# Kernel tuning notes

Measured on AMD Instinct MI355X. Metric: run time of the kernel, lower is better.

The kernel has to match this reference:

```python
import jax, jax.numpy as jnp
import numpy as np

HOP = 512
FAC = 4
FRAME_LEN = FAC * HOP  # 2048
ALPHA = 0.65
BETA = 0.06


def _inverse_stft_window():
    # torch.hann_window (periodic): w[n] = 0.5*(1 - cos(2*pi*n/N))
    n = np.arange(FRAME_LEN)
    w = 0.5 * (1.0 - np.cos(2.0 * np.pi * n / FRAME_LEN))
    denom = w ** 2
    # overlaps = ceil(frame_length / hop) == FAC (frame_length = FAC*HOP exactly)
    denom = denom.reshape(FAC, HOP).sum(axis=0)          # [HOP]
    denom = np.tile(denom, FAC)                          # [FRAME_LEN]
    return (w / denom).astype(np.float32)


def setup_inputs() -> dict:
    key = jax.random.key(0)
    B, F, T = 8, 1024, 2048
    stft_frames = jax.random.normal(key, (B, 2, F, T), dtype=jnp.float32)
    inv_window = jnp.asarray(_inverse_stft_window())
    return {"stft_frames": stft_frames, "inv_window": inv_window}


def reference(stft_frames, inv_window):
    # stft_frames: [B, 2, F, T] (real/imag stacked on dim 1)
    x = jnp.pad(stft_frames, ((0, 0), (0, 0), (0, 1), (0, 0)))  # F -> F+1 (Nyquist bin)
    real = x[:, 0] / BETA   # [B, F+1, T]
    imag = x[:, 1] / BETA
    # denormalize_complex: |x|^(1/alpha) * exp(i * atan2(im, re))
    mag = (real * real + imag * imag) ** (0.5 / ALPHA)
    theta = jnp.arctan2(imag, real)
    spec = jax.lax.complex(mag * jnp.cos(theta), mag * jnp.sin(theta))  # [B, F+1, T]
    frames = jnp.fft.irfft(spec, axis=-2)                 # [B, 2F, T], 2F == FRAME_LEN
    frames = jnp.transpose(frames, (0, 2, 1))             # [B, T, L]
    frames = frames * inv_window[None, None, :]
    B, T, L = frames.shape
    total = (T - 1) * HOP + L
    # vectorized overlap-add (scatter-add replacing the per-frame python loop)
    idx = (jnp.arange(T)[:, None] * HOP + jnp.arange(L)[None, :]).reshape(-1)  # [T*L]
    full = jnp.zeros((B, total), frames.dtype).at[:, idx].add(frames.reshape(B, -1))
    # output_buffer is empty on the first call; chunk = first hop*T samples
    return full[:, : HOP * T]
```

## Files before the change

### kernel.cpp

```cpp
#include <hip/hip_runtime.h>
#include <cstddef>


#define TDIM 2048
#define FDIM 1024
#define TT 8
#define NTOT (512 * 2048)
#define SPLANE 4224

static constexpr int kBREV[32] = {0,16,8,24,4,20,12,28,2,18,10,26,6,22,14,30,
                                  1,17,9,25,5,21,13,29,3,19,11,27,7,23,15,31};
static constexpr float kTR[16] = {
  1.0f, 0.98078528040323044f, 0.92387953251128674f, 0.83146961230254524f,
  0.70710678118654757f, 0.55557023301960218f, 0.38268343236508978f, 0.19509032201612825f,
  0.0f, -0.19509032201612825f, -0.38268343236508978f, -0.55557023301960218f,
  -0.70710678118654757f, -0.83146961230254524f, -0.92387953251128674f, -0.98078528040323044f};
static constexpr float kTI[16] = {
  0.0f, 0.19509032201612825f, 0.38268343236508978f, 0.55557023301960218f,
  0.70710678118654757f, 0.83146961230254524f, 0.92387953251128674f, 0.98078528040323044f,
  1.0f, 0.98078528040323044f, 0.92387953251128674f, 0.83146961230254524f,
  0.70710678118654757f, 0.55557023301960218f, 0.38268343236508978f, 0.19509032201612825f};
static constexpr float kCC[32] = {
  1.0f, 0.99518472667219693f, 0.98078528040323044f, 0.95694033573220882f,
  0.92387953251128674f, 0.88192126434835505f, 0.83146961230254524f, 0.77301045336273699f,
  0.70710678118654757f, 0.63439328416364549f, 0.55557023301960218f, 0.47139673682599764f,
  0.38268343236508978f, 0.29028467725446233f, 0.19509032201612825f, 0.098017140329560604f,
  0.0f, -0.098017140329560604f, -0.19509032201612825f, -0.29028467725446233f,
  -0.38268343236508978f, -0.47139673682599764f, -0.55557023301960218f, -0.63439328416364549f,
  -0.70710678118654757f, -0.77301045336273699f, -0.83146961230254524f, -0.88192126434835505f,
  -0.92387953251128674f, -0.95694033573220882f, -0.98078528040323044f, -0.99518472667219693f};
static constexpr float kSS[32] = {
  0.0f, 0.098017140329560604f, 0.19509032201612825f, 0.29028467725446233f,
  0.38268343236508978f, 0.47139673682599764f, 0.55557023301960218f, 0.63439328416364549f,
  0.70710678118654757f, 0.77301045336273699f, 0.83146961230254524f, 0.88192126434835505f,
  0.92387953251128674f, 0.95694033573220882f, 0.98078528040323044f, 0.99518472667219693f,
  1.0f, 0.99518472667219693f, 0.98078528040323044f, 0.95694033573220882f,
  0.92387953251128674f, 0.88192126434835505f, 0.83146961230254524f, 0.77301045336273699f,
  0.70710678118654757f, 0.63439328416364549f, 0.55557023301960218f, 0.47139673682599764f,
  0.38268343236508978f, 0.29028467725446233f, 0.19509032201612825f, 0.098017140329560604f};

template <int H>
__device__ __forceinline__ void fft32_stage(float ar[32], float ai[32]) {
  constexpr int TSTEP = 16 / H;
  #pragma unroll
  for (int g = 0; g < 32; g += 2 * H) {
    #pragma unroll
    for (int j = 0; j < H; ++j) {
      const float twr = kTR[j * TSTEP];
      const float twi = kTI[j * TSTEP];
      const int i0 = g + j, i1 = i0 + H;
      const float tr = twr * ar[i1] - twi * ai[i1];
      const float ti = twr * ai[i1] + twi * ar[i1];
      ar[i1] = ar[i0] - tr; ai[i1] = ai[i0] - ti;
      ar[i0] += tr;         ai[i0] += ti;
    }
  }
}

__device__ __forceinline__ void ifft32_core(float ar[32], float ai[32]) {
  fft32_stage<1>(ar, ai);
  fft32_stage<2>(ar, ai);
  fft32_stage<4>(ar, ai);
  fft32_stage<8>(ar, ai);
  fft32_stage<16>(ar, ai);
}

__device__ __forceinline__ float pow_gain(float v, float PE, float KS) {
  return KS * __builtin_amdgcn_exp2f(PE * __builtin_amdgcn_logf(v));
}

__device__ __forceinline__ void denorm4(float4& r, float4& i, float PE, float KS) {
  float g;
  g = pow_gain(r.x * r.x + i.x * i.x, PE, KS); r.x *= g; i.x *= g;
  g = pow_gain(r.y * r.y + i.y * i.y, PE, KS); r.y *= g; i.y *= g;
  g = pow_gain(r.z * r.z + i.z * i.z, PE, KS); r.z *= g; i.z *= g;
  g = pow_gain(r.w * r.w + i.w * i.w, PE, KS); r.w *= g; i.w *= g;
}

template <int SC>
__device__ __forceinline__ int slot_row(int s) {
  return (SC == 0) ? (s < 256 ? s : s + 512) : (s + 256);
}

template <int SC>
__device__ __forceinline__ void stage1_compute(const float* __restrict__ Sre,
                                               const float* __restrict__ Sim,
                                               int q, int tl, float wc, float ws,
                                               float ar[32], float ai[32]) {
  #pragma unroll
  for (int u = 0; u < 16; ++u) {
    const int k2 = (SC == 0) ? (u < 8 ? u : u + 16) : (u + 8);
    const int slot = q + 32 * u;
    int slotm_zero = 32 * (16 - u);
    if (SC == 0 && u == 0) slotm_zero = 0;
    if (SC == 0 && u == 8) slotm_zero = 512;
    const int slotm_pos = (32 - q) + 32 * (15 - u);
    const int slotm = (q == 0) ? slotm_zero : slotm_pos;

    const float s1r = Sre[slot * 8 + tl],  s1i = Sim[slot * 8 + tl];
    const float s2r = Sre[slotm * 8 + tl], s2i = Sim[slotm * 8 + tl];
    const float cs = wc * kCC[k2] - ws * kSS[k2];
    const float sn = ws * kCC[k2] + wc * kSS[k2];
    const float Pre = s1r + s2r, Pim = s1i - s2i;
    const float Qre = s1r - s2r, Qim = s1i + s2i;
    const float uu = cs * Qim + sn * Qre;
    const float vv = cs * Qre - sn * Qim;
    float wr = Pre - uu, wi = Pim + vv;
    if (q == 0 && k2 == 0) { wr = s1r; wi = s1r; }
    ar[kBREV[k2]] = wr; ai[kBREV[k2]] = wi;
  }
}

#define XIDX(t, k1, r) ((k1) * 264 + (r) * 8 + (t))
#define FSTR 2054

__global__ __launch_bounds__(256) void istft_fused(const float* __restrict__ in,
                                                   const float* __restrict__ invw,
                                                   float* __restrict__ out) {
  __shared__ float buf[16896];
  float* Sre = buf;
  float* Sim = buf + SPLANE;
  float* Xr  = buf;
  float* Xi  = buf + 8448;
  float* Fh  = buf;

  const int tid = threadIdx.x;
  const int tl  = tid & 7;
  const int q   = tid >> 3;

  const int id   = blockIdx.x;
  const int xcd  = id & 7;
  const int slot = id >> 3;
  const int b    = slot >> 5;
  const int tile = xcd * 32 + (slot & 31);
  const int t0   = tile * TT;

  const float* re_p = in + ((size_t)b * 2 + 0) * ((size_t)FDIM * TDIM);
  const float* im_p = in + ((size_t)b * 2 + 1) * ((size_t)FDIM * TDIM);

  const float KS = (float)(exp((-1.0 / 0.65) * log(0.06)) / 2048.0);
  const float PE = 7.0f / 26.0f;

  const float aq = 3.0679615757712824e-3f * (float)q;
  const float wc = __cosf(aq), ws = __sinf(aq);

  float ar[32], ai[32];

  {
    float4 reA[4], imA[4];
    #pragma unroll
    for (int j = 0; j < 4; ++j) {
      const int f = tid + 256 * j;
      const int s = f >> 1, cg = f & 1;
      const int row = slot_row<0>(s);
      reA[j] = *(const float4*)(re_p + (size_t)row * TDIM + t0 + 4 * cg);
      imA[j] = *(const float4*)(im_p + (size_t)row * TDIM + t0 + 4 * cg);
    }
    float4 exRe, exIm;
    if (tid < 2) {
      exRe = *(const float4*)(re_p + (size_t)256 * TDIM + t0 + 4 * tid);
      exIm = *(const float4*)(im_p + (size_t)256 * TDIM + t0 + 4 * tid);
    }
    #pragma unroll
    for (int j = 0; j < 4; ++j) {
      const int f = tid + 256 * j;
      const int s = f >> 1, cg = f & 1;
      denorm4(reA[j], imA[j], PE, KS);
      *(float4*)(Sre + s * 8 + 4 * cg) = reA[j];
      *(float4*)(Sim + s * 8 + 4 * cg) = imA[j];
    }
    if (tid < 2) {
      denorm4(exRe, exIm, PE, KS);
      *(float4*)(Sre + 512 * 8 + 4 * tid) = exRe;
      *(float4*)(Sim + 512 * 8 + 4 * tid) = exIm;
    }

    float4 reB[4], imB[4];
    #pragma unroll
    for (int j = 0; j < 4; ++j) {
      const int f = tid + 256 * j;
      const int s = f >> 1, cg = f & 1;
      const int row = slot_row<1>(s);
      reB[j] = *(const float4*)(re_p + (size_t)row * TDIM + t0 + 4 * cg);
      imB[j] = *(const float4*)(im_p + (size_t)row * TDIM + t0 + 4 * cg);
    }
    float4 exReB, exImB;
    if (tid < 2) {
      exReB = *(const float4*)(re_p + (size_t)768 * TDIM + t0 + 4 * tid);
      exImB = *(const float4*)(im_p + (size_t)768 * TDIM + t0 + 4 * tid);
    }
    __syncthreads();

    stage1_compute<0>(Sre, Sim, q, tl, wc, ws, ar, ai);
    __syncthreads();

    #pragma unroll
    for (int j = 0; j < 4; ++j) {
      const int f = tid + 256 * j;
      const int s = f >> 1, cg = f & 1;
      denorm4(reB[j], imB[j], PE, KS);
      *(float4*)(Sre + s * 8 + 4 * cg) = reB[j];
      *(float4*)(Sim + s * 8 + 4 * cg) = imB[j];
    }
    if (tid < 2) {
      denorm4(exReB, exImB, PE, KS);
      *(float4*)(Sre + 512 * 8 + 4 * tid) = exReB;
      *(float4*)(Sim + 512 * 8 + 4 * tid) = exImB;
    }
    __syncthreads();
    stage1_compute<1>(Sre, Sim, q, tl, wc, ws, ar, ai);
    __syncthreads();
  }

  ifft32_core(ar, ai);

  {
    const float aq2 = 6.1359231515425649e-3f * (float)q;
    const float dc = __cosf(aq2), dsn = __sinf(aq2);
    float cs = 1.0f, sn = 0.0f;
    #pragma unroll
    for (int r = 0; r < 32; ++r) {
      Xr[XIDX(tl, q, r)] = cs * ar[r] - sn * ai[r];
      Xi[XIDX(tl, q, r)] = cs * ai[r] + sn * ar[r];
      const float ncs = cs * dc - sn * dsn;
      sn = cs * dsn + sn * dc;
      cs = ncs;
    }
  }
  __syncthreads();
  float zr[32], zi[32];
  #pragma unroll
  for (int i = 0; i < 32; ++i) {
    zr[i] = Xr[XIDX(tl, kBREV[i], q)];
    zi[i] = Xi[XIDX(tl, kBREV[i], q)];
  }
  __syncthreads();

  ifft32_core(zr, zi);

  #pragma unroll
  for (int s = 0; s < 32; ++s) {
    const int l0 = 2 * q + 64 * s;
    const float2 w2 = *(const float2*)(invw + l0);
    float2 fv; fv.x = zr[s] * w2.x; fv.y = zi[s] * w2.y;
    *(float2*)(Fh + tl * FSTR + l0) = fv;
  }
  __syncthreads();

  float* ob = out + (size_t)b * NTOT;
  for (int rel = 0; rel < 11; ++rel) {
    const int tp = t0 + rel;
    if (tp > 2047) break;
    #pragma unroll
    for (int half = 0; half < 2; ++half) {
      const int j = tid + 256 * half;
      float v = 0.0f;
      #pragma unroll
      for (int c = 0; c < 4; ++c) {
        const int tt = rel - c;
        if (tt >= 0 && tt < TT) v += Fh[tt * FSTR + j + 512 * c];
      }
      const int n = tp * 512 + j;
      if (rel >= 3 && rel <= 7) ob[n] = v;
      else atomicAdd(&ob[n], v);
    }
  }
}

extern "C" void kernel_launch(void* const* d_in, const int* in_sizes, int n_in,
                              void* d_out, int out_size, void* d_ws, size_t ws_size,
                              hipStream_t stream) {
  (void)in_sizes; (void)n_in; (void)d_ws; (void)ws_size;
  const float* in   = (const float*)d_in[0];
  const float* invw = (const float*)d_in[1];
  float* out = (float*)d_out;
  hipMemsetAsync(out, 0, (size_t)out_size * sizeof(float), stream);
  istft_fused<<<dim3(TDIM / TT * 8), 256, 0, stream>>>(in, invw, out);
}
```

Before: 229.6 us.

## Compute real-IFFT pre-twiddle pairs at load time and store interleaved in LDS

The Hermitian pair combination (P/Q with the pre-twiddle rotation) now runs in the loading threads, which hold both mirrored bins k and N-k. Each pair yields both outputs, so the twiddle math is done once per pair. The result goes into shared memory as interleaved complex values with a padded stride, and the FFT threads read one float2 per element instead of four scalar loads plus the rotation. In exchange the slot assignment and DC/Nyquist special cases become more intricate. The per-thread twiddle changes from per-element constant-table products to __cosf/__sinf per pair.

```diff
diff --git a/kernel.cpp b/kernel.cpp
--- a/kernel.cpp
+++ b/kernel.cpp
@@ -6,7 +6,7 @@
 #define FDIM 1024
 #define TT 8
 #define NTOT (512 * 2048)
-#define SPLANE 4224
+#define SSTR 20
 
 static constexpr int kBREV[32] = {0,16,8,24,4,20,12,28,2,18,10,26,6,22,14,30,
                                   1,17,9,25,5,21,13,29,3,19,11,27,7,23,15,31};
@@ -20,24 +20,6 @@
   0.70710678118654757f, 0.83146961230254524f, 0.92387953251128674f, 0.98078528040323044f,
   1.0f, 0.98078528040323044f, 0.92387953251128674f, 0.83146961230254524f,
   0.70710678118654757f, 0.55557023301960218f, 0.38268343236508978f, 0.19509032201612825f};
-static constexpr float kCC[32] = {
-  1.0f, 0.99518472667219693f, 0.98078528040323044f, 0.95694033573220882f,
-  0.92387953251128674f, 0.88192126434835505f, 0.83146961230254524f, 0.77301045336273699f,
-  0.70710678118654757f, 0.63439328416364549f, 0.55557023301960218f, 0.47139673682599764f,
-  0.38268343236508978f, 0.29028467725446233f, 0.19509032201612825f, 0.098017140329560604f,
-  0.0f, -0.098017140329560604f, -0.19509032201612825f, -0.29028467725446233f,
-  -0.38268343236508978f, -0.47139673682599764f, -0.55557023301960218f, -0.63439328416364549f,
-  -0.70710678118654757f, -0.77301045336273699f, -0.83146961230254524f, -0.88192126434835505f,
-  -0.92387953251128674f, -0.95694033573220882f, -0.98078528040323044f, -0.99518472667219693f};
-static constexpr float kSS[32] = {
-  0.0f, 0.098017140329560604f, 0.19509032201612825f, 0.29028467725446233f,
-  0.38268343236508978f, 0.47139673682599764f, 0.55557023301960218f, 0.63439328416364549f,
-  0.70710678118654757f, 0.77301045336273699f, 0.83146961230254524f, 0.88192126434835505f,
-  0.92387953251128674f, 0.95694033573220882f, 0.98078528040323044f, 0.99518472667219693f,
-  1.0f, 0.99518472667219693f, 0.98078528040323044f, 0.95694033573220882f,
-  0.92387953251128674f, 0.88192126434835505f, 0.83146961230254524f, 0.77301045336273699f,
-  0.70710678118654757f, 0.63439328416364549f, 0.55557023301960218f, 0.47139673682599764f,
-  0.38268343236508978f, 0.29028467725446233f, 0.19509032201612825f, 0.098017140329560604f};
 
 template <int H>
 __device__ __forceinline__ void fft32_stage(float ar[32], float ai[32]) {
@@ -82,32 +64,46 @@
   return (SC == 0) ? (s < 256 ? s : s + 512) : (s + 256);
 }
 
+__device__ __forceinline__ void pack_pair_store(float* __restrict__ Sri,
+    int sa, int sb, int cg, const float4& ar_, const float4& ai_,
+    const float4& br_, const float4& bi_, int rowa) {
+  const float ang = 3.0679615757712824e-3f * (float)rowa;
+  const float ca = __cosf(ang), sn = __sinf(ang);
+  const float arr[4] = {ar_.x, ar_.y, ar_.z, ar_.w};
+  const float aii[4] = {ai_.x, ai_.y, ai_.z, ai_.w};
+  const float brr[4] = {br_.x, br_.y, br_.z, br_.w};
+  const float bii[4] = {bi_.x, bi_.y, bi_.z, bi_.w};
+  float wa[8], wb[8];
+  #pragma unroll
+  for (int t = 0; t < 4; ++t) {
+    const float Pre = arr[t] + brr[t], Pim = aii[t] - bii[t];
+    const float Qre = arr[t] - brr[t], Qim = aii[t] + bii[t];
+    const float u = ca * Qim + sn * Qre;
+    const float v = ca * Qre - sn * Qim;
+    wa[2*t] = Pre - u; wa[2*t+1] = Pim + v;
+    wb[2*t] = Pre + u; wb[2*t+1] = v - Pim;
+  }
+  *(float4*)(Sri + sa * SSTR + 8 * cg)     = make_float4(wa[0], wa[1], wa[2], wa[3]);
+  *(float4*)(Sri + sa * SSTR + 8 * cg + 4) = make_float4(wa[4], wa[5], wa[6], wa[7]);
+  *(float4*)(Sri + sb * SSTR + 8 * cg)     = make_float4(wb[0], wb[1], wb[2], wb[3]);
+  *(float4*)(Sri + sb * SSTR + 8 * cg + 4) = make_float4(wb[4], wb[5], wb[6], wb[7]);
+}
+
+__device__ __forceinline__ void dc_store(float* __restrict__ Sri, int cg,
+                                         const float4& r) {
+  *(float4*)(Sri + 8 * cg)     = make_float4(r.x, r.x, r.y, r.y);
+  *(float4*)(Sri + 8 * cg + 4) = make_float4(r.z, r.z, r.w, r.w);
+}
+
 template <int SC>
-__device__ __forceinline__ void stage1_compute(const float* __restrict__ Sre,
-                                               const float* __restrict__ Sim,
-                                               int q, int tl, float wc, float ws,
-                                               float ar[32], float ai[32]) {
+__device__ __forceinline__ void stage1_read(const float* __restrict__ Sri,
+                                            int q, int tl,
+                                            float ar[32], float ai[32]) {
   #pragma unroll
   for (int u = 0; u < 16; ++u) {
     const int k2 = (SC == 0) ? (u < 8 ? u : u + 16) : (u + 8);
-    const int slot = q + 32 * u;
-    int slotm_zero = 32 * (16 - u);
-    if (SC == 0 && u == 0) slotm_zero = 0;
-    if (SC == 0 && u == 8) slotm_zero = 512;
-    const int slotm_pos = (32 - q) + 32 * (15 - u);
-    const int slotm = (q == 0) ? slotm_zero : slotm_pos;
-
-    const float s1r = Sre[slot * 8 + tl],  s1i = Sim[slot * 8 + tl];
-    const float s2r = Sre[slotm * 8 + tl], s2i = Sim[slotm * 8 + tl];
-    const float cs = wc * kCC[k2] - ws * kSS[k2];
-    const float sn = ws * kCC[k2] + wc * kSS[k2];
-    const float Pre = s1r + s2r, Pim = s1i - s2i;
-    const float Qre = s1r - s2r, Qim = s1i + s2i;
-    const float uu = cs * Qim + sn * Qre;
-    const float vv = cs * Qre - sn * Qim;
-    float wr = Pre - uu, wi = Pim + vv;
-    if (q == 0 && k2 == 0) { wr = s1r; wi = s1r; }
-    ar[kBREV[k2]] = wr; ai[kBREV[k2]] = wi;
+    const float2 w = *(const float2*)(Sri + (q + 32 * u) * SSTR + 2 * tl);
+    ar[kBREV[k2]] = w.x; ai[kBREV[k2]] = w.y;
   }
 }
 
@@ -118,8 +114,7 @@
                                                    const float* __restrict__ invw,
                                                    float* __restrict__ out) {
   __shared__ float buf[16896];
-  float* Sre = buf;
-  float* Sim = buf + SPLANE;
+  float* Sri = buf;
   float* Xr  = buf;
   float* Xi  = buf + 8448;
   float* Fh  = buf;
@@ -141,8 +136,11 @@
   const float KS = (float)(exp((-1.0 / 0.65) * log(0.06)) / 2048.0);
   const float PE = 7.0f / 26.0f;
 
-  const float aq = 3.0679615757712824e-3f * (float)q;
-  const float wc = __cosf(aq), ws = __sinf(aq);
+  const int c  = tid >> 1;
+  const int cg = tid & 1;
+  int s_[4];
+  if (c) { s_[0] = c; s_[1] = 512 - c; s_[2] = 128 + c; s_[3] = 384 - c; }
+  else   { s_[0] = 0; s_[1] = 256;     s_[2] = 128;     s_[3] = 384;     }
 
   float ar[32], ai[32];
 
@@ -150,65 +148,57 @@
     float4 reA[4], imA[4];
     #pragma unroll
     for (int j = 0; j < 4; ++j) {
-      const int f = tid + 256 * j;
-      const int s = f >> 1, cg = f & 1;
-      const int row = slot_row<0>(s);
+      const int row = slot_row<0>(s_[j]);
       reA[j] = *(const float4*)(re_p + (size_t)row * TDIM + t0 + 4 * cg);
       imA[j] = *(const float4*)(im_p + (size_t)row * TDIM + t0 + 4 * cg);
     }
-    float4 exRe, exIm;
+    float4 exR, exI;
     if (tid < 2) {
-      exRe = *(const float4*)(re_p + (size_t)256 * TDIM + t0 + 4 * tid);
-      exIm = *(const float4*)(im_p + (size_t)256 * TDIM + t0 + 4 * tid);
-    }
+      exR = *(const float4*)(re_p + (size_t)256 * TDIM + t0 + 4 * tid);
+      exI = *(const float4*)(im_p + (size_t)256 * TDIM + t0 + 4 * tid);
+    }
+    #pragma unroll
+    for (int j = 0; j < 4; ++j) denorm4(reA[j], imA[j], PE, KS);
+    if (tid < 2) denorm4(exR, exI, PE, KS);
+    if (c) {
+      pack_pair_store(Sri, s_[0], s_[1], cg, reA[0], imA[0], reA[1], imA[1], c);
+      pack_pair_store(Sri, s_[2], s_[3], cg, reA[2], imA[2], reA[3], imA[3], 128 + c);
+    } else {
+      dc_store(Sri, cg, reA[0]);
+      pack_pair_store(Sri, 128, 384, cg, reA[2], imA[2], reA[3], imA[3], 128);
+      pack_pair_store(Sri, 256, 512, cg, reA[1], imA[1], exR, exI, 768);
+    }
+
+    float4 reB[4], imB[4];
     #pragma unroll
     for (int j = 0; j < 4; ++j) {
-      const int f = tid + 256 * j;
-      const int s = f >> 1, cg = f & 1;
-      denorm4(reA[j], imA[j], PE, KS);
-      *(float4*)(Sre + s * 8 + 4 * cg) = reA[j];
-      *(float4*)(Sim + s * 8 + 4 * cg) = imA[j];
-    }
-    if (tid < 2) {
-      denorm4(exRe, exIm, PE, KS);
-      *(float4*)(Sre + 512 * 8 + 4 * tid) = exRe;
-      *(float4*)(Sim + 512 * 8 + 4 * tid) = exIm;
-    }
-
-    float4 reB[4], imB[4];
-    #pragma unroll
-    for (int j = 0; j < 4; ++j) {
-      const int f = tid + 256 * j;
-      const int s = f >> 1, cg = f & 1;
-      const int row = slot_row<1>(s);
+      const int row = slot_row<1>(s_[j]);
       reB[j] = *(const float4*)(re_p + (size_t)row * TDIM + t0 + 4 * cg);
       imB[j] = *(const float4*)(im_p + (size_t)row * TDIM + t0 + 4 * cg);
     }
-    float4 exReB, exImB;
+    float4 exRB, exIB;
     if (tid < 2) {
-      exReB = *(const float4*)(re_p + (size_t)768 * TDIM + t0 + 4 * tid);
-      exImB = *(const float4*)(im_p + (size_t)768 * TDIM + t0 + 4 * tid);
-    }
-    __syncthreads();
-
-    stage1_compute<0>(Sre, Sim, q, tl, wc, ws, ar, ai);
-    __syncthreads();
-
-    #pragma unroll
-    for (int j = 0; j < 4; ++j) {
-      const int f = tid + 256 * j;
-      const int s = f >> 1, cg = f & 1;
-      denorm4(reB[j], imB[j], PE, KS);
-      *(float4*)(Sre + s * 8 + 4 * cg) = reB[j];
-      *(float4*)(Sim + s * 8 + 4 * cg) = imB[j];
-    }
-    if (tid < 2) {
-      denorm4(exReB, exImB, PE, KS);
-      *(float4*)(Sre + 512 * 8 + 4 * tid) = exReB;
-      *(float4*)(Sim + 512 * 8 + 4 * tid) = exImB;
-    }
-    __syncthreads();
-    stage1_compute<1>(Sre, Sim, q, tl, wc, ws, ar, ai);
+      exRB = *(const float4*)(re_p + (size_t)768 * TDIM + t0 + 4 * tid);
+      exIB = *(const float4*)(im_p + (size_t)768 * TDIM + t0 + 4 * tid);
+    }
+    __syncthreads();
+
+    stage1_read<0>(Sri, q, tl, ar, ai);
+    __syncthreads();
+
+    #pragma unroll
+    for (int j = 0; j < 4; ++j) denorm4(reB[j], imB[j], PE, KS);
+    if (tid < 2) denorm4(exRB, exIB, PE, KS);
+    if (c) {
+      pack_pair_store(Sri, s_[0], s_[1], cg, reB[0], imB[0], reB[1], imB[1], 256 + c);
+      pack_pair_store(Sri, s_[2], s_[3], cg, reB[2], imB[2], reB[3], imB[3], 384 + c);
+    } else {
+      pack_pair_store(Sri, 0, 512, cg, reB[0], imB[0], exRB, exIB, 256);
+      pack_pair_store(Sri, 128, 384, cg, reB[2], imB[2], reB[3], imB[3], 384);
+      pack_pair_store(Sri, 256, 256, cg, reB[1], imB[1], reB[1], imB[1], 512);
+    }
+    __syncthreads();
+    stage1_read<1>(Sri, q, tl, ar, ai);
     __syncthreads();
   }
 
@@ -256,9 +246,9 @@
       const int j = tid + 256 * half;
       float v = 0.0f;
       #pragma unroll
-      for (int c = 0; c < 4; ++c) {
-        const int tt = rel - c;
-        if (tt >= 0 && tt < TT) v += Fh[tt * FSTR + j + 512 * c];
+      for (int cc = 0; cc < 4; ++cc) {
+        const int tt = rel - cc;
+        if (tt >= 0 && tt < TT) v += Fh[tt * FSTR + j + 512 * cc];
       }
       const int n = tp * 512 + j;
       if (rel >= 3 && rel <= 7) ob[n] = v;
```

After: 228.9 us. No clear change (-0.3%).
